# Kernel tuning notes

Measured on AMD Instinct MI355X. Metric: run time of the kernel, lower is better.

Reference implementation:

```python
import jax, jax.numpy as jnp
import numpy as np

N_NODES = 50000
N_EDGES = 800000
N_FEAT = 128
HID = 128
N_LAYER = 3
FC_HID = 256
N_CLASS = 10
N_GRAPHS = 64


def setup_inputs() -> dict:
    key = jax.random.key(0)
    ks = jax.random.split(key, 10)
    x = jax.random.normal(ks[0], (N_NODES, N_FEAT), dtype=jnp.float32)
    edge_index = jax.random.randint(ks[1], (2, N_EDGES), 0, N_NODES, dtype=jnp.int32)
    batch = jnp.sort(jax.random.randint(ks[2], (N_NODES,), 0, N_GRAPHS, dtype=jnp.int32))
    s = 0.05
    # SAGEConv per layer: lin_l acts on mean-aggregated neighbors, lin_r on root.
    Wl = jax.random.normal(ks[3], (N_LAYER, HID, HID), dtype=jnp.float32) * s
    Wr = jax.random.normal(ks[4], (N_LAYER, HID, HID), dtype=jnp.float32) * s
    bl = jnp.zeros((N_LAYER, HID), dtype=jnp.float32)
    fc1_w = jax.random.normal(ks[5], (HID * N_LAYER, FC_HID), dtype=jnp.float32) * s
    fc1_b = jnp.zeros((FC_HID,), dtype=jnp.float32)
    fc2_w = jax.random.normal(ks[6], (FC_HID, N_CLASS), dtype=jnp.float32) * s
    fc2_b = jnp.zeros((N_CLASS,), dtype=jnp.float32)
    return {"x": x, "edge_index": edge_index, "batch": batch,
            "Wl": Wl, "Wr": Wr, "bl": bl,
            "fc1_w": fc1_w, "fc1_b": fc1_b, "fc2_w": fc2_w, "fc2_b": fc2_b}


def reference(x, edge_index, batch, Wl, Wr, bl, fc1_w, fc1_b, fc2_w, fc2_b):
    # normalize edge indices to start at 0 (as in the torch forward)
    ei = edge_index - jnp.min(edge_index)
    src, dst = ei[0], ei[1]
    # in-degree for mean aggregation (clamped to avoid div-by-zero)
    deg = jax.ops.segment_sum(jnp.ones((src.shape[0],), x.dtype), dst,
                              num_segments=N_NODES)
    inv_deg = 1.0 / jnp.maximum(deg, 1.0)[:, None]  # [N,1]
    h = x
    layer_outs = []
    for i in range(N_LAYER):
        # (dropout is identity in eval mode)
        agg = jax.ops.segment_sum(h[src], dst, num_segments=N_NODES) * inv_deg  # [N,H]
        h = jax.nn.relu(agg @ Wl[i] + h @ Wr[i] + bl[i])
        layer_outs.append(h)
    hcat = jnp.concatenate(layer_outs, axis=1)  # [N, H*n_layer]
    # mean pooling per graph
    counts = jax.ops.segment_sum(jnp.ones((N_NODES,), x.dtype), batch,
                                 num_segments=N_GRAPHS)
    pooled = jax.ops.segment_sum(hcat, batch, num_segments=N_GRAPHS)
    pooled = pooled / jnp.maximum(counts, 1.0)[:, None]  # [G, H*n_layer]
    out = jax.nn.relu(pooled @ fc1_w + fc1_b) @ fc2_w + fc2_b  # [G, n_class]
    return out
```

## Files before the change

### kernel.cpp

```cpp
#include <hip/hip_runtime.h>
#include <hip/hip_bf16.h>
#include <limits.h>

#define N_NODES 50000
#define N_EDGES 800000
#define HID 128
#define N_LAYER 3
#define FC_HID 256
#define N_CLASS 10
#define N_GRAPHS 64
#define NBKT 98
#define BIN_NB 256
#define PER_BLK ((N_EDGES + BIN_NB - 1) / BIN_NB)

typedef __attribute__((ext_vector_type(8))) short short8;
typedef __attribute__((ext_vector_type(4))) float f32x4;

__device__ inline unsigned f2bf(float f) {
    unsigned u = __float_as_uint(f);
    return (u + 0x7FFFu + ((u >> 16) & 1u)) >> 16;
}

__global__ __launch_bounds__(512) void k_minh(
    const int* __restrict__ ei, const float* __restrict__ x,
    const float* __restrict__ Wl, const float* __restrict__ Wr,
    int* __restrict__ bmin, int* __restrict__ hist, unsigned* __restrict__ xb,
    unsigned* __restrict__ wlh, unsigned* __restrict__ wrh) {
    __shared__ int red[512];
    __shared__ int lh[NBKT];
    const int b = blockIdx.x, t = threadIdx.x;
    if (t < NBKT) lh[t] = 0;
    __syncthreads();
    int e0 = b * PER_BLK, e1 = min(e0 + PER_BLK, N_EDGES);
    int v = INT_MAX;
    for (int j = e0 + t; j < e1; j += 512) {
        int s = ei[j], d = ei[N_EDGES + j];
        v = min(v, min(s, d));
        atomicAdd(&lh[d >> 9], 1);
    }
    for (int i = b * 512 + t; i < N_NODES * HID / 4; i += BIN_NB * 512) {
        float4 xv = *(const float4*)(x + (size_t)i * 4);
        uint2 o;
        o.x = f2bf(xv.x) | (f2bf(xv.y) << 16);
        o.y = f2bf(xv.z) | (f2bf(xv.w) << 16);
        *(uint2*)(xb + (size_t)i * 2) = o;
    }
    if (b >= 250) {
        int w = b - 250;
        const float* src = (w < 3) ? (Wl + (size_t)w * HID * HID)
                                   : (Wr + (size_t)(w - 3) * HID * HID);
        unsigned* dh = (w < 3) ? (wlh + (size_t)w * HID * 64) : (wrh + (size_t)(w - 3) * HID * 64);
        for (int i = 0; i < 16; ++i) {
            int u = t * 16 + i;
            int n = u >> 6, kk = u & 63;
            float v0 = src[(size_t)(2 * kk) * HID + n];
            float v1 = src[(size_t)(2 * kk + 1) * HID + n];
            dh[u] = f2bf(v0) | (f2bf(v1) << 16);
        }
    }
    red[t] = v;
    __syncthreads();
    for (int off = 256; off > 0; off >>= 1) {
        if (t < off) red[t] = min(red[t], red[t + off]);
        __syncthreads();
    }
    if (t == 0) bmin[b] = red[0];
    if (t < NBKT) hist[b * NBKT + t] = lh[t];
}

__global__ void k_base(const int* __restrict__ hist, int* __restrict__ colex,
                       int* __restrict__ btot, float* __restrict__ pooled,
                       const int* __restrict__ bmin, int* __restrict__ emin,
                       const int* __restrict__ batch, float* __restrict__ counts) {
    __shared__ int s[BIN_NB];
    __shared__ int s2[BIN_NB];
    const int b = blockIdx.x, t = threadIdx.x;
    int gid = b * BIN_NB + t;
    if (gid < N_GRAPHS * HID * N_LAYER) pooled[gid] = 0.f;
    int v = hist[t * NBKT + b];
    s[t] = v;
    __syncthreads();
    for (int off = 1; off < BIN_NB; off <<= 1) {
        int u = (t >= off) ? s[t - off] : 0;
        __syncthreads();
        s[t] += u;
        __syncthreads();
    }
    colex[t * NBKT + b] = s[t] - v;
    if (t == BIN_NB - 1) btot[b] = s[t];
    if (b == 0) {
        s2[t] = bmin[t];
        __syncthreads();
        for (int off = 128; off > 0; off >>= 1) {
            if (t < off) s2[t] = min(s2[t], s2[t + off]);
            __syncthreads();
        }
        if (t == 0) *emin = s2[0];
        if (t < N_GRAPHS) {
            int g = t;
            int lo = 0, hi = N_NODES;
            while (lo < hi) { int mid = (lo + hi) >> 1; if (batch[mid] < g) lo = mid + 1; else hi = mid; }
            int lb = lo;
            lo = lb; hi = N_NODES;
            while (lo < hi) { int mid = (lo + hi) >> 1; if (batch[mid] <= g) lo = mid + 1; else hi = mid; }
            counts[g] = (float)(lo - lb);
        }
    }
}

__global__ __launch_bounds__(512) void k_bin(const int* __restrict__ ei,
                                             const int* __restrict__ emin,
                                             const int* __restrict__ btot,
                                             const int* __restrict__ colex,
                                             unsigned* __restrict__ ebuf) {
    __shared__ int sb[128];
    __shared__ int lcnt[NBKT];
    __shared__ int lbase[NBKT];
    const int t = threadIdx.x, blk = blockIdx.x;
    int v = (t < NBKT) ? btot[t] : 0;
    if (t < 128) sb[t] = v;
    __syncthreads();
    for (int off = 1; off < 128; off <<= 1) {
        int u = (t >= off && t < 128) ? sb[t - off] : 0;
        __syncthreads();
        if (t < 128) sb[t] += u;
        __syncthreads();
    }
    if (t < NBKT) {
        lcnt[t] = 0;
        lbase[t] = (sb[t] - v) + colex[blk * NBKT + t];
    }
    __syncthreads();
    int m = *emin;
    int e0 = blk * PER_BLK, e1 = min(e0 + PER_BLK, N_EDGES);
    for (int j = e0 + t; j < e1; j += 512) {
        int s = ei[j] - m, d = ei[N_EDGES + j];
        int bk = d >> 9;
        int idx = atomicAdd(&lcnt[bk], 1);
        ebuf[lbase[bk] + idx] = ((unsigned)s << 9) | (unsigned)(d & 511);
    }
}

__global__ __launch_bounds__(512) void k_scatter2(const unsigned* __restrict__ ebuf,
                                                  const int* __restrict__ btot,
                                                  const int* __restrict__ emin,
                                                  int* __restrict__ rp,
                                                  float* __restrict__ invd,
                                                  int* __restrict__ csr) {
    __shared__ int ldeg[512];
    __shared__ int lsc[512];
    __shared__ int lfill[512];
    __shared__ int bbsh[NBKT + 1];
    const int b = blockIdx.x, t = threadIdx.x;
    int v = (t < NBKT) ? btot[t] : 0;
    if (t < 128) ldeg[t] = v;
    __syncthreads();
    for (int off = 1; off < 128; off <<= 1) {
        int u = (t >= off && t < 128) ? ldeg[t - off] : 0;
        __syncthreads();
        if (t < 128) ldeg[t] += u;
        __syncthreads();
    }
    if (t < NBKT) bbsh[t] = ldeg[t] - v;
    if (t == 127) bbsh[NBKT] = ldeg[127];
    __syncthreads();
    int m = *emin;
    if (b == NBKT) {
        if (t == 0) rp[N_NODES] = bbsh[NBKT];
        for (int nd = NBKT * 512 - m + t; nd < N_NODES; nd += 512)
            if (nd >= 0) { rp[nd] = N_EDGES; invd[nd] = 1.0f; }
        return;
    }
    int beg = bbsh[b], end = bbsh[b + 1];
    ldeg[t] = 0;
    lfill[t] = 0;
    __syncthreads();
    for (int e = beg + t; e < end; e += 512)
        atomicAdd(&ldeg[ebuf[e] & 511], 1);
    __syncthreads();
    int dv = ldeg[t];
    lsc[t] = dv;
    __syncthreads();
    for (int off = 1; off < 512; off <<= 1) {
        int u = (t >= off) ? lsc[t - off] : 0;
        __syncthreads();
        lsc[t] += u;
        __syncthreads();
    }
    int base = beg + lsc[t] - dv;
    lsc[t] = base;
    int nd = (b << 9) + t - m;
    if (nd >= 0 && nd < N_NODES) {
        rp[nd] = base;
        invd[nd] = 1.0f / (float)max(dv, 1);
    }
    __syncthreads();
    for (int e = beg + t; e < end; e += 512) {
        unsigned p = ebuf[e];
        int loc = p & 511;
        int pos = lsc[loc] + atomicAdd(&lfill[loc], 1);
        csr[pos] = (int)(p >> 9);
    }
}

__global__ void k_agg(const unsigned* __restrict__ hb, const int* __restrict__ rp,
                      const int* __restrict__ csr, const float* __restrict__ invd,
                      unsigned* __restrict__ aggb) {
    const int n = blockIdx.x;
    const int lane = threadIdx.x;
    int beg = rp[n], end = rp[n + 1];
    float a0 = 0, a1 = 0, b0 = 0, b1 = 0, c0 = 0, c1 = 0, d0 = 0, d1 = 0;
    int e = beg;
    for (; e + 16 <= end; e += 16) {
        int s[16];
        unsigned u[16];
#pragma unroll
        for (int i = 0; i < 16; ++i) s[i] = csr[e + i];
#pragma unroll
        for (int i = 0; i < 16; ++i) u[i] = hb[(size_t)s[i] * 64 + lane];
#pragma unroll
        for (int i = 0; i < 16; i += 4) {
            a0 += __uint_as_float(u[i] << 16);     a1 += __uint_as_float(u[i] & 0xFFFF0000u);
            b0 += __uint_as_float(u[i + 1] << 16); b1 += __uint_as_float(u[i + 1] & 0xFFFF0000u);
            c0 += __uint_as_float(u[i + 2] << 16); c1 += __uint_as_float(u[i + 2] & 0xFFFF0000u);
            d0 += __uint_as_float(u[i + 3] << 16); d1 += __uint_as_float(u[i + 3] & 0xFFFF0000u);
        }
    }
    for (; e + 4 <= end; e += 4) {
        int s0 = csr[e], s1 = csr[e + 1], s2 = csr[e + 2], s3 = csr[e + 3];
        unsigned u0 = hb[(size_t)s0 * 64 + lane];
        unsigned u1 = hb[(size_t)s1 * 64 + lane];
        unsigned u2 = hb[(size_t)s2 * 64 + lane];
        unsigned u3 = hb[(size_t)s3 * 64 + lane];
        a0 += __uint_as_float(u0 << 16); a1 += __uint_as_float(u0 & 0xFFFF0000u);
        b0 += __uint_as_float(u1 << 16); b1 += __uint_as_float(u1 & 0xFFFF0000u);
        c0 += __uint_as_float(u2 << 16); c1 += __uint_as_float(u2 & 0xFFFF0000u);
        d0 += __uint_as_float(u3 << 16); d1 += __uint_as_float(u3 & 0xFFFF0000u);
    }
    for (; e < end; ++e) {
        unsigned u = hb[(size_t)csr[e] * 64 + lane];
        a0 += __uint_as_float(u << 16);
        a1 += __uint_as_float(u & 0xFFFF0000u);
    }
    float iv = invd[n];
    unsigned o = f2bf((a0 + b0 + c0 + d0) * iv) | (f2bf((a1 + b1 + c1 + d1) * iv) << 16);
    aggb[(size_t)n * 64 + lane] = o;
}

__global__ __launch_bounds__(256, 4) void k_gemm(
    const unsigned* __restrict__ aggb, const unsigned* __restrict__ hinb,
    const unsigned* __restrict__ wlh, const unsigned* __restrict__ wrh,
    const float* __restrict__ bias, const int* __restrict__ batch,
    unsigned* __restrict__ houtb, float* __restrict__ pooled, int layer, int store_h) {
    __shared__ float Ts[64 * 132];
    __shared__ int bs[64];
    const int tx = threadIdx.x;
    const int wave = tx >> 6, lane = tx & 63;
    const int row0 = blockIdx.x * 64;
    const int lrow = lane & 15, kgrp = lane >> 4;

    if (tx < 64) {
        int grow = row0 + tx;
        bs[tx] = (grow < N_NODES) ? batch[grow] : -1;
    }

    f32x4 acc[4][2];
#pragma unroll
    for (int m = 0; m < 4; ++m)
#pragma unroll
        for (int n = 0; n < 2; ++n) acc[m][n] = (f32x4){0.f, 0.f, 0.f, 0.f};
    const short8 zf = {0, 0, 0, 0, 0, 0, 0, 0};

    for (int kc = 0; kc < 4; ++kc) {
        const int koff = kc * 16 + kgrp * 4;
        short8 af[4], hf[4];
#pragma unroll
        for (int m = 0; m < 4; ++m) {
            int r = row0 + m * 16 + lrow;
            if (r < N_NODES) {
                af[m] = *(const short8*)(aggb + (size_t)r * 64 + koff);
                hf[m] = *(const short8*)(hinb + (size_t)r * 64 + koff);
            } else {
                af[m] = zf;
                hf[m] = zf;
            }
        }
#pragma unroll
        for (int n = 0; n < 2; ++n) {
            int wn = wave * 2 + n;
            size_t wbase = (size_t)(wn * 16 + lrow) * 64 + koff;
            short8 fl = *(const short8*)(wlh + wbase);
            short8 fr = *(const short8*)(wrh + wbase);
#pragma unroll
            for (int m = 0; m < 4; ++m) {
                acc[m][n] = __builtin_amdgcn_mfma_f32_16x16x32_bf16(af[m], fl, acc[m][n], 0, 0, 0);
                acc[m][n] = __builtin_amdgcn_mfma_f32_16x16x32_bf16(hf[m], fr, acc[m][n], 0, 0, 0);
            }
        }
    }

#pragma unroll
    for (int n = 0; n < 2; ++n) {
        int c = wave * 32 + n * 16 + lrow;
        float bb = bias[c];
#pragma unroll
        for (int m = 0; m < 4; ++m)
#pragma unroll
            for (int reg = 0; reg < 4; ++reg) {
                int r = m * 16 + kgrp * 4 + reg;
                Ts[r * 132 + c] = fmaxf(acc[m][n][reg] + bb, 0.f);
            }
    }
    __syncthreads();

    if (store_h) {
#pragma unroll
        for (int it = 0; it < 4; ++it) {
            int f = it * 256 + tx;
            int r = f >> 4, slot = f & 15;
            int grow = row0 + r;
            if (grow < N_NODES) {
                const float* ts = &Ts[r * 132 + slot * 8];
                uint4 o;
                o.x = f2bf(ts[0]) | (f2bf(ts[1]) << 16);
                o.y = f2bf(ts[2]) | (f2bf(ts[3]) << 16);
                o.z = f2bf(ts[4]) | (f2bf(ts[5]) << 16);
                o.w = f2bf(ts[6]) | (f2bf(ts[7]) << 16);
                *(uint4*)(houtb + (size_t)grow * 64 + slot * 4) = o;
            }
        }
    }

    {
        int j = tx & 127, half = tx >> 7;
        int rbeg = half * 32, rend = rbeg + 32;
        float run = 0.f;
        int curb = bs[rbeg];
        for (int r = rbeg; r < rend; ++r) {
            int bb = bs[r];
            if (bb != curb) {
                if (curb >= 0)
                    atomicAdd(&pooled[(size_t)curb * (HID * N_LAYER) + layer * HID + j], run);
                run = 0.f;
                curb = bb;
            }
            run += Ts[r * 132 + j];
        }
        if (curb >= 0)
            atomicAdd(&pooled[(size_t)curb * (HID * N_LAYER) + layer * HID + j], run);
    }
}

__global__ void k_fc(const float* __restrict__ pooled, const float* __restrict__ counts,
                     const float* __restrict__ fc1w, const float* __restrict__ fc1b,
                     const float* __restrict__ fc2w, const float* __restrict__ fc2b,
                     float* __restrict__ out) {
    __shared__ float pr[HID * N_LAYER];
    __shared__ float a1[FC_HID];
    const int g = blockIdx.x, t = threadIdx.x;
    float invc = 1.0f / fmaxf(counts[g], 1.0f);
    for (int i = t; i < HID * N_LAYER; i += FC_HID)
        pr[i] = pooled[(size_t)g * (HID * N_LAYER) + i] * invc;
    __syncthreads();
    float acc = fc1b[t];
    for (int k = 0; k < HID * N_LAYER; ++k)
        acc = fmaf(pr[k], fc1w[(size_t)k * FC_HID + t], acc);
    a1[t] = fmaxf(acc, 0.f);
    __syncthreads();
    if (t < N_CLASS) {
        float o = fc2b[t];
        for (int k = 0; k < FC_HID; ++k)
            o = fmaf(a1[k], fc2w[(size_t)k * N_CLASS + t], o);
        out[(size_t)g * N_CLASS + t] = o;
    }
}

extern "C" void kernel_launch(void* const* d_in, const int* in_sizes, int n_in,
                              void* d_out, int out_size, void* d_ws, size_t ws_size,
                              hipStream_t stream) {
    const float* x = (const float*)d_in[0];
    const int* ei = (const int*)d_in[1];
    const int* batch = (const int*)d_in[2];
    const float* Wl = (const float*)d_in[3];
    const float* Wr = (const float*)d_in[4];
    const float* bl = (const float*)d_in[5];
    const float* fc1w = (const float*)d_in[6];
    const float* fc1b = (const float*)d_in[7];
    const float* fc2w = (const float*)d_in[8];
    const float* fc2b = (const float*)d_in[9];
    float* out = (float*)d_out;

    char* ws = (char*)d_ws;
    size_t off = 0;
    auto alloc = [&](size_t bytes) {
        void* p = ws + off;
        off += (bytes + 255) & ~size_t(255);
        return p;
    };
    int* emin = (int*)alloc(4);
    int* bmin = (int*)alloc(BIN_NB * 4);
    float* pooled = (float*)alloc((size_t)N_GRAPHS * HID * N_LAYER * 4);
    int* hist = (int*)alloc((size_t)BIN_NB * NBKT * 4);
    int* colex = (int*)alloc((size_t)BIN_NB * NBKT * 4);
    int* btot = (int*)alloc(NBKT * 4);
    int* rp = (int*)alloc((N_NODES + 1) * 4);
    float* invd = (float*)alloc(N_NODES * 4);
    float* counts = (float*)alloc(N_GRAPHS * 4);
    unsigned* ebuf = (unsigned*)alloc((size_t)N_EDGES * 4);
    int* csr = (int*)alloc((size_t)N_EDGES * 4);
    unsigned* wlh = (unsigned*)alloc((size_t)N_LAYER * HID * 64 * 4);
    unsigned* wrh = (unsigned*)alloc((size_t)N_LAYER * HID * 64 * 4);
    unsigned* aggb = (unsigned*)alloc((size_t)N_NODES * 64 * 4);
    unsigned* xb = (unsigned*)alloc((size_t)N_NODES * 64 * 4);
    unsigned* hb1 = (unsigned*)alloc((size_t)N_NODES * 64 * 4);
    unsigned* hb2 = (unsigned*)alloc((size_t)N_NODES * 64 * 4);

    k_minh<<<BIN_NB, 512, 0, stream>>>(ei, x, Wl, Wr, bmin, hist, xb, wlh, wrh);
    k_base<<<NBKT, BIN_NB, 0, stream>>>(hist, colex, btot, pooled, bmin, emin, batch, counts);
    k_bin<<<BIN_NB, 512, 0, stream>>>(ei, emin, btot, colex, ebuf);
    k_scatter2<<<NBKT + 1, 512, 0, stream>>>(ebuf, btot, emin, rp, invd, csr);

    const unsigned* hin = xb;
    unsigned* houts[3] = {hb1, hb2, hb1};
    for (int layer = 0; layer < N_LAYER; ++layer) {
        k_agg<<<N_NODES, 64, 0, stream>>>(hin, rp, csr, invd, aggb);
        k_gemm<<<(N_NODES + 63) / 64, 256, 0, stream>>>(
            aggb, hin,
            wlh + (size_t)layer * HID * 64, wrh + (size_t)layer * HID * 64,
            bl + (size_t)layer * HID, batch, houts[layer], pooled, layer,
            layer < N_LAYER - 1 ? 1 : 0);
        hin = houts[layer];
    }
    k_fc<<<N_GRAPHS, 256, 0, stream>>>(pooled, counts, fc1w, fc1b, fc2w, fc2b, out);
}
```

Before: 225.0 us.

## Eliminate k_base kernel by recomputing scans in consumers; prefetch GEMM operand fragments

Result: slower. 234.3 us (+4.1%).

```diff
diff --git a/kernel.cpp b/kernel.cpp
--- a/kernel.cpp
+++ b/kernel.cpp
@@ -25,12 +25,15 @@
     const int* __restrict__ ei, const float* __restrict__ x,
     const float* __restrict__ Wl, const float* __restrict__ Wr,
     int* __restrict__ bmin, int* __restrict__ hist, unsigned* __restrict__ xb,
-    unsigned* __restrict__ wlh, unsigned* __restrict__ wrh) {
+    unsigned* __restrict__ wlh, unsigned* __restrict__ wrh,
+    float* __restrict__ pooled) {
     __shared__ int red[512];
     __shared__ int lh[NBKT];
     const int b = blockIdx.x, t = threadIdx.x;
     if (t < NBKT) lh[t] = 0;
     __syncthreads();
+    int gid = b * 512 + t;
+    if (gid < N_GRAPHS * HID * N_LAYER) pooled[gid] = 0.f;
     int e0 = b * PER_BLK, e1 = min(e0 + PER_BLK, N_EDGES);
     int v = INT_MAX;
     for (int j = e0 + t; j < e1; j += 512) {
@@ -38,7 +41,7 @@
         v = min(v, min(s, d));
         atomicAdd(&lh[d >> 9], 1);
     }
-    for (int i = b * 512 + t; i < N_NODES * HID / 4; i += BIN_NB * 512) {
+    for (int i = gid; i < N_NODES * HID / 4; i += BIN_NB * 512) {
         float4 xv = *(const float4*)(x + (size_t)i * 4);
         uint2 o;
         o.x = f2bf(xv.x) | (f2bf(xv.y) << 16);
@@ -68,70 +71,43 @@
     if (t < NBKT) hist[b * NBKT + t] = lh[t];
 }
 
-__global__ void k_base(const int* __restrict__ hist, int* __restrict__ colex,
-                       int* __restrict__ btot, float* __restrict__ pooled,
-                       const int* __restrict__ bmin, int* __restrict__ emin,
-                       const int* __restrict__ batch, float* __restrict__ counts) {
-    __shared__ int s[BIN_NB];
-    __shared__ int s2[BIN_NB];
-    const int b = blockIdx.x, t = threadIdx.x;
-    int gid = b * BIN_NB + t;
-    if (gid < N_GRAPHS * HID * N_LAYER) pooled[gid] = 0.f;
-    int v = hist[t * NBKT + b];
-    s[t] = v;
-    __syncthreads();
-    for (int off = 1; off < BIN_NB; off <<= 1) {
-        int u = (t >= off) ? s[t - off] : 0;
-        __syncthreads();
-        s[t] += u;
-        __syncthreads();
-    }
-    colex[t * NBKT + b] = s[t] - v;
-    if (t == BIN_NB - 1) btot[b] = s[t];
-    if (b == 0) {
-        s2[t] = bmin[t];
-        __syncthreads();
-        for (int off = 128; off > 0; off >>= 1) {
-            if (t < off) s2[t] = min(s2[t], s2[t + off]);
-            __syncthreads();
-        }
-        if (t == 0) *emin = s2[0];
-        if (t < N_GRAPHS) {
-            int g = t;
-            int lo = 0, hi = N_NODES;
-            while (lo < hi) { int mid = (lo + hi) >> 1; if (batch[mid] < g) lo = mid + 1; else hi = mid; }
-            int lb = lo;
-            lo = lb; hi = N_NODES;
-            while (lo < hi) { int mid = (lo + hi) >> 1; if (batch[mid] <= g) lo = mid + 1; else hi = mid; }
-            counts[g] = (float)(lo - lb);
-        }
-    }
-}
-
 __global__ __launch_bounds__(512) void k_bin(const int* __restrict__ ei,
-                                             const int* __restrict__ emin,
-                                             const int* __restrict__ btot,
-                                             const int* __restrict__ colex,
+                                             const int* __restrict__ bmin,
+                                             const int* __restrict__ hist,
                                              unsigned* __restrict__ ebuf) {
-    __shared__ int sb[128];
+    __shared__ int smin[256];
+    __shared__ int sscan[128];
     __shared__ int lcnt[NBKT];
     __shared__ int lbase[NBKT];
     const int t = threadIdx.x, blk = blockIdx.x;
-    int v = (t < NBKT) ? btot[t] : 0;
-    if (t < 128) sb[t] = v;
+    if (t < 256) smin[t] = bmin[t];
+    __syncthreads();
+    for (int off = 128; off > 0; off >>= 1) {
+        if (t < off) smin[t] = min(smin[t], smin[t + off]);
+        __syncthreads();
+    }
+    int tot = 0, cx = 0;
+    if (t < NBKT) {
+        for (int j = 0; j < BIN_NB; ++j) {
+            int h = hist[j * NBKT + t];
+            tot += h;
+            cx += (j < blk) ? h : 0;
+        }
+    }
+    if (t < 128) sscan[t] = tot;
     __syncthreads();
     for (int off = 1; off < 128; off <<= 1) {
-        int u = (t >= off && t < 128) ? sb[t - off] : 0;
-        __syncthreads();
-        if (t < 128) sb[t] += u;
+        int u = (t >= off && t < 128) ? sscan[t - off] : 0;
+        __syncthreads();
+        if (t < 128) sscan[t] += u;
         __syncthreads();
     }
     if (t < NBKT) {
         lcnt[t] = 0;
-        lbase[t] = (sb[t] - v) + colex[blk * NBKT + t];
-    }
-    __syncthreads();
-    int m = *emin;
+        lbase[t] = (sscan[t] - tot) + cx;
+    }
+    __syncthreads();
+    int m = smin[0];
     int e0 = blk * PER_BLK, e1 = min(e0 + PER_BLK, N_EDGES);
     for (int j = e0 + t; j < e1; j += 512) {
         int s = ei[j] - m, d = ei[N_EDGES + j];
@@ -142,8 +118,8 @@
 }
 
 __global__ __launch_bounds__(512) void k_scatter2(const unsigned* __restrict__ ebuf,
-                                                  const int* __restrict__ btot,
-                                                  const int* __restrict__ emin,
+                                                  const int* __restrict__ bmin,
+                                                  const int* __restrict__ hist,
                                                   int* __restrict__ rp,
                                                   float* __restrict__ invd,
                                                   int* __restrict__ csr) {
@@ -151,20 +127,30 @@
     __shared__ int lsc[512];
     __shared__ int lfill[512];
     __shared__ int bbsh[NBKT + 1];
+    __shared__ int smin[256];
     const int b = blockIdx.x, t = threadIdx.x;
-    int v = (t < NBKT) ? btot[t] : 0;
-    if (t < 128) ldeg[t] = v;
+    if (t < 256) smin[t] = bmin[t];
+    __syncthreads();
+    for (int off = 128; off > 0; off >>= 1) {
+        if (t < off) smin[t] = min(smin[t], smin[t + off]);
+        __syncthreads();
+    }
+    int tot = 0;
+    if (t < NBKT) {
+        for (int j = 0; j < BIN_NB; ++j) tot += hist[j * NBKT + t];
+    }
+    if (t < 128) lsc[t] = tot;
     __syncthreads();
     for (int off = 1; off < 128; off <<= 1) {
-        int u = (t >= off && t < 128) ? ldeg[t - off] : 0;
-        __syncthreads();
-        if (t < 128) ldeg[t] += u;
-        __syncthreads();
-    }
-    if (t < NBKT) bbsh[t] = ldeg[t] - v;
-    if (t == 127) bbsh[NBKT] = ldeg[127];
-    __syncthreads();
-    int m = *emin;
+        int u = (t >= off && t < 128) ? lsc[t - off] : 0;
+        __syncthreads();
+        if (t < 128) lsc[t] += u;
+        __syncthreads();
+    }
+    if (t < NBKT) bbsh[t] = lsc[t] - tot;
+    if (t == 127) bbsh[NBKT] = lsc[127];
+    __syncthreads();
+    int m = smin[0];
     if (b == NBKT) {
         if (t == 0) rp[N_NODES] = bbsh[NBKT];
         for (int nd = NBKT * 512 - m + t; nd < N_NODES; nd += 512)
@@ -271,20 +257,36 @@
         for (int n = 0; n < 2; ++n) acc[m][n] = (f32x4){0.f, 0.f, 0.f, 0.f};
     const short8 zf = {0, 0, 0, 0, 0, 0, 0, 0};
 
+    short8 af[4], hf[4], afn[4], hfn[4];
+    const int koff0 = kgrp * 4;
+#pragma unroll
+    for (int m = 0; m < 4; ++m) {
+        int r = row0 + m * 16 + lrow;
+        if (r < N_NODES) {
+            af[m] = *(const short8*)(aggb + (size_t)r * 64 + koff0);
+            hf[m] = *(const short8*)(hinb + (size_t)r * 64 + koff0);
+        } else {
+            af[m] = zf;
+            hf[m] = zf;
+        }
+    }
+#pragma unroll
     for (int kc = 0; kc < 4; ++kc) {
+        if (kc < 3) {
+            const int koffn = (kc + 1) * 16 + kgrp * 4;
+#pragma unroll
+            for (int m = 0; m < 4; ++m) {
+                int r = row0 + m * 16 + lrow;
+                if (r < N_NODES) {
+                    afn[m] = *(const short8*)(aggb + (size_t)r * 64 + koffn);
+                    hfn[m] = *(const short8*)(hinb + (size_t)r * 64 + koffn);
+                } else {
+                    afn[m] = zf;
+                    hfn[m] = zf;
+                }
+            }
+        }
         const int koff = kc * 16 + kgrp * 4;
-        short8 af[4], hf[4];
-#pragma unroll
-        for (int m = 0; m < 4; ++m) {
-            int r = row0 + m * 16 + lrow;
-            if (r < N_NODES) {
-                af[m] = *(const short8*)(aggb + (size_t)r * 64 + koff);
-                hf[m] = *(const short8*)(hinb + (size_t)r * 64 + koff);
-            } else {
-                af[m] = zf;
-                hf[m] = zf;
-            }
-        }
 #pragma unroll
         for (int n = 0; n < 2; ++n) {
             int wn = wave * 2 + n;
@@ -296,6 +298,10 @@
                 acc[m][n] = __builtin_amdgcn_mfma_f32_16x16x32_bf16(af[m], fl, acc[m][n], 0, 0, 0);
                 acc[m][n] = __builtin_amdgcn_mfma_f32_16x16x32_bf16(hf[m], fr, acc[m][n], 0, 0, 0);
             }
+        }
+        if (kc < 3) {
+#pragma unroll
+            for (int m = 0; m < 4; ++m) { af[m] = afn[m]; hf[m] = hfn[m]; }
         }
     }
 
@@ -351,14 +357,24 @@
     }
 }
 
-__global__ void k_fc(const float* __restrict__ pooled, const float* __restrict__ counts,
+__global__ void k_fc(const float* __restrict__ pooled, const int* __restrict__ batch,
                      const float* __restrict__ fc1w, const float* __restrict__ fc1b,
                      const float* __restrict__ fc2w, const float* __restrict__ fc2b,
                      float* __restrict__ out) {
     __shared__ float pr[HID * N_LAYER];
     __shared__ float a1[FC_HID];
+    __shared__ float invc_sh;
     const int g = blockIdx.x, t = threadIdx.x;
-    float invc = 1.0f / fmaxf(counts[g], 1.0f);
+    if (t == 0) {
+        int lo = 0, hi = N_NODES;
+        while (lo < hi) { int mid = (lo + hi) >> 1; if (batch[mid] < g) lo = mid + 1; else hi = mid; }
+        int lb = lo;
+        lo = lb; hi = N_NODES;
+        while (lo < hi) { int mid = (lo + hi) >> 1; if (batch[mid] <= g) lo = mid + 1; else hi = mid; }
+        invc_sh = 1.0f / fmaxf((float)(lo - lb), 1.0f);
+    }
+    __syncthreads();
+    float invc = invc_sh;
     for (int i = t; i < HID * N_LAYER; i += FC_HID)
         pr[i] = pooled[(size_t)g * (HID * N_LAYER) + i] * invc;
     __syncthreads();
@@ -397,15 +413,11 @@
         off += (bytes + 255) & ~size_t(255);
         return p;
     };
-    int* emin = (int*)alloc(4);
     int* bmin = (int*)alloc(BIN_NB * 4);
     float* pooled = (float*)alloc((size_t)N_GRAPHS * HID * N_LAYER * 4);
     int* hist = (int*)alloc((size_t)BIN_NB * NBKT * 4);
-    int* colex = (int*)alloc((size_t)BIN_NB * NBKT * 4);
-    int* btot = (int*)alloc(NBKT * 4);
     int* rp = (int*)alloc((N_NODES + 1) * 4);
     float* invd = (float*)alloc(N_NODES * 4);
-    float* counts = (float*)alloc(N_GRAPHS * 4);
     unsigned* ebuf = (unsigned*)alloc((size_t)N_EDGES * 4);
     int* csr = (int*)alloc((size_t)N_EDGES * 4);
     unsigned* wlh = (unsigned*)alloc((size_t)N_LAYER * HID * 64 * 4);
@@ -415,10 +427,9 @@
     unsigned* hb1 = (unsigned*)alloc((size_t)N_NODES * 64 * 4);
     unsigned* hb2 = (unsigned*)alloc((size_t)N_NODES * 64 * 4);
 
-    k_minh<<<BIN_NB, 512, 0, stream>>>(ei, x, Wl, Wr, bmin, hist, xb, wlh, wrh);
-    k_base<<<NBKT, BIN_NB, 0, stream>>>(hist, colex, btot, pooled, bmin, emin, batch, counts);
-    k_bin<<<BIN_NB, 512, 0, stream>>>(ei, emin, btot, colex, ebuf);
-    k_scatter2<<<NBKT + 1, 512, 0, stream>>>(ebuf, btot, emin, rp, invd, csr);
+    k_minh<<<BIN_NB, 512, 0, stream>>>(ei, x, Wl, Wr, bmin, hist, xb, wlh, wrh, pooled);
+    k_bin<<<BIN_NB, 512, 0, stream>>>(ei, bmin, hist, ebuf);
+    k_scatter2<<<NBKT + 1, 512, 0, stream>>>(ebuf, bmin, hist, rp, invd, csr);
 
     const unsigned* hin = xb;
     unsigned* houts[3] = {hb1, hb2, hb1};
@@ -431,5 +442,5 @@
             layer < N_LAYER - 1 ? 1 : 0);
         hin = houts[layer];
     }
-    k_fc<<<N_GRAPHS, 256, 0, stream>>>(pooled, counts, fc1w, fc1b, fc2w, fc2b, out);
-}
+    k_fc<<<N_GRAPHS, 256, 0, stream>>>(pooled, batch, fc1w, fc1b, fc2w, fc2b, out);
+}
```
